# Kernel optimization log

Measured on AMD Instinct MI355X. Metric: run time of the kernel, lower is better.

## Reference

```python
import jax, jax.numpy as jnp
import numpy as np

EMBED_DIM = 1024
NUM_HEADS = 16
HEAD_DIM = EMBED_DIM // NUM_HEADS
BSZ, SEQ = 2, 2048


def setup_inputs() -> dict:
    key = jax.random.key(0)
    ks = jax.random.split(key, 7)
    s = 0.02  # keep logits in a sane range
    return {
        "hidden_states": jax.random.normal(ks[0], (BSZ, SEQ, EMBED_DIM), jnp.float32),
        "attention_mask": jnp.zeros((1, 1, SEQ, SEQ), jnp.float32),
        "q_w": jax.random.normal(ks[1], (2 * EMBED_DIM, EMBED_DIM), jnp.float32) * s,
        "q_b": jnp.zeros((2 * EMBED_DIM,), jnp.float32),
        "k_w": jax.random.normal(ks[2], (EMBED_DIM, EMBED_DIM), jnp.float32) * s,
        "k_b": jnp.zeros((EMBED_DIM,), jnp.float32),
        "v_w": jax.random.normal(ks[3], (EMBED_DIM, EMBED_DIM), jnp.float32) * s,
        "v_b": jnp.zeros((EMBED_DIM,), jnp.float32),
        "o_w": jax.random.normal(ks[4], (EMBED_DIM, EMBED_DIM), jnp.float32) * s,
        "o_b": jnp.zeros((EMBED_DIM,), jnp.float32),
    }


def reference(hidden_states, attention_mask, q_w, q_b, k_w, k_b, v_w, v_b, o_w, o_b):
    bsz, seq, _ = hidden_states.shape
    h, d = NUM_HEADS, HEAD_DIM
    inv_sqrt_d = 1.0 / np.sqrt(d).astype(np.float32)

    qg = hidden_states @ q_w.T + q_b                      # [b, s, 2*h*d]
    q, gate_logits = jnp.split(qg, [h * d], axis=-1)       # elementwise gate
    k = hidden_states @ k_w.T + k_b
    v = hidden_states @ v_w.T + v_b

    q = q.reshape(bsz, seq, h, d).transpose(0, 2, 1, 3)    # [b, h, s, d]
    k = k.reshape(bsz, seq, h, d).transpose(0, 2, 1, 3)
    v = v.reshape(bsz, seq, h, d).transpose(0, 2, 1, 3)

    scores = jnp.einsum("bhqd,bhkd->bhqk", q, k) * inv_sqrt_d
    scores = scores + attention_mask
    weights = jax.nn.softmax(scores, axis=-1)
    attn = jnp.einsum("bhqk,bhkd->bhqd", weights, v)       # [b, h, s, d]

    gate = jax.nn.sigmoid(gate_logits.reshape(bsz, seq, h, d).transpose(0, 2, 1, 3))
    attn = attn * gate

    attn = attn.transpose(0, 2, 1, 3).reshape(bsz, seq, h * d)
    return attn @ o_w.T + o_b
```

## Files before the change

kernel.cpp:

```cpp
#include <hip/hip_runtime.h>
#include <cstdint>
#include <cstddef>

#define AS1 __attribute__((address_space(1)))
#define AS3 __attribute__((address_space(3)))

typedef __bf16 bf16x8 __attribute__((ext_vector_type(8)));
typedef __bf16 bf16x4 __attribute__((ext_vector_type(4)));
typedef float  f32x4  __attribute__((ext_vector_type(4)));
typedef float  f32x16 __attribute__((ext_vector_type(16)));
typedef unsigned int u32x4 __attribute__((ext_vector_type(4)));

#define MFMA_BF16(a, b, c) __builtin_amdgcn_mfma_f32_16x16x32_bf16((a), (b), (c), 0, 0, 0)
#define MFMA32(a, b, c)    __builtin_amdgcn_mfma_f32_32x32x16_bf16((a), (b), (c), 0, 0, 0)

__device__ __forceinline__ void gload16(const __bf16* g, __bf16* l) {
  __builtin_amdgcn_global_load_lds((AS1 void*)(uintptr_t)g, (AS3 void*)l, 16, 0, 0);
}

__device__ __forceinline__ unsigned int cvtpk_bf16(float lo, float hi) {
  unsigned int r;
  asm("v_cvt_pk_bf16_f32 %0, %1, %2" : "=v"(r) : "v"(lo), "v"(hi));
  return r;
}

__device__ __forceinline__ void permswap(unsigned int& a, unsigned int& b) {
  asm volatile("v_permlane32_swap_b32 %0, %1" : "+v"(a), "+v"(b));
}

__global__ void cvt_all_kernel(
    const float* __restrict__ hs, const float* __restrict__ qw, const float* __restrict__ kw,
    const float* __restrict__ vw, const float* __restrict__ ow,
    __bf16* __restrict__ Xb, __bf16* __restrict__ qwb, __bf16* __restrict__ kwb,
    __bf16* __restrict__ vwb, __bf16* __restrict__ owb,
    const unsigned long long* __restrict__ mask, int* __restrict__ flag)
{
  const int gid = blockIdx.x * blockDim.x + threadIdx.x;
  const int stride = gridDim.x * blockDim.x;
  for (int i = gid; i < 1179648; i += stride) {
    const float* s; __bf16* d; int o;
    if (i < 524288)       { s = hs; d = Xb;  o = i; }
    else if (i < 786432)  { s = qw; d = qwb; o = i - 524288; }
    else if (i < 917504)  { s = kw; d = kwb; o = i - 786432; }
    else if (i < 1048576) { s = vw; d = vwb; o = i - 917504; }
    else                  { s = ow; d = owb; o = i - 1048576; }
    const float4* p = (const float4*)(s + (size_t)o * 8);
    float4 a = p[0], b = p[1];
    bf16x8 v;
    v[0] = (__bf16)a.x; v[1] = (__bf16)a.y; v[2] = (__bf16)a.z; v[3] = (__bf16)a.w;
    v[4] = (__bf16)b.x; v[5] = (__bf16)b.y; v[6] = (__bf16)b.z; v[7] = (__bf16)b.w;
    *(bf16x8*)(d + (size_t)o * 8) = v;
  }
  bool nz = false;
  for (int i = gid; i < 2097152; i += stride) nz |= (mask[i] != 0ull);
  if (nz) atomicOr(flag, 1);
}

__global__ __launch_bounds__(256) void proj_kernel(
    const __bf16* __restrict__ X,
    const __bf16* __restrict__ qw, const float* __restrict__ qb,
    const __bf16* __restrict__ kw, const float* __restrict__ kb,
    const __bf16* __restrict__ vw, const float* __restrict__ vb,
    __bf16* __restrict__ Qo, __bf16* __restrict__ Ko,
    __bf16* __restrict__ VTo, __bf16* __restrict__ Go)
{
  __shared__ __bf16 As[2][128][64];
  __shared__ __bf16 Bs[2][128][64];

  const int bid = blockIdx.x;
  const int r = bid >> 3;
  const int ntile = (bid & 7) * 4 + (r >> 5);
  const int mtile = r & 31;
  const int m0 = mtile * 128;
  const int n0 = ntile * 128;

  const __bf16* W; const float* bias; int nb;
  if (n0 < 2048)      { W = qw; bias = qb; nb = n0; }
  else if (n0 < 3072) { W = kw; bias = kb; nb = n0 - 2048; }
  else                { W = vw; bias = vb; nb = n0 - 3072; }

  const int tid = threadIdx.x;
  const int wv = tid >> 6, ln = tid & 63;
  const int wr = wv >> 1, wc = wv & 1;
  const int qr = ln & 15, qg = ln >> 4;
  const int lrow = ln >> 3, lcol = (ln & 7) * 8;

  f32x4 acc[4][4];
#pragma unroll
  for (int m = 0; m < 4; ++m)
#pragma unroll
    for (int n = 0; n < 4; ++n) acc[m][n] = 0.f;

  __bf16 (*Asc)[64] = As[0], (*Asn)[64] = As[1];
  __bf16 (*Bsc)[64] = Bs[0], (*Bsn)[64] = Bs[1];

#pragma unroll
  for (int i = 0; i < 4; ++i) {
    const int rb = i * 32 + wv * 8;
    gload16(X + (size_t)(m0 + rb + lrow) * 1024 + lcol, &Asc[rb][0]);
    gload16(W + (size_t)(nb + rb + lrow) * 1024 + lcol, &Bsc[rb][0]);
  }
  __syncthreads();

  for (int t = 0; t < 16; ++t) {
    if (t < 15) {
      const int k0 = (t + 1) * 64;
#pragma unroll
      for (int i = 0; i < 4; ++i) {
        const int rb = i * 32 + wv * 8;
        gload16(X + (size_t)(m0 + rb + lrow) * 1024 + k0 + lcol, &Asn[rb][0]);
        gload16(W + (size_t)(nb + rb + lrow) * 1024 + k0 + lcol, &Bsn[rb][0]);
      }
    }
#pragma unroll
    for (int kk = 0; kk < 2; ++kk) {
      bf16x8 af[4], bfv[4];
#pragma unroll
      for (int m = 0; m < 4; ++m) af[m] = *(const bf16x8*)&Asc[wr * 64 + m * 16 + qr][kk * 32 + qg * 8];
#pragma unroll
      for (int n = 0; n < 4; ++n) bfv[n] = *(const bf16x8*)&Bsc[wc * 64 + n * 16 + qr][kk * 32 + qg * 8];
#pragma unroll
      for (int m = 0; m < 4; ++m)
#pragma unroll
        for (int n = 0; n < 4; ++n) acc[m][n] = MFMA_BF16(af[m], bfv[n], acc[m][n]);
    }
    __syncthreads();
    __bf16 (*ta)[64] = Asc; Asc = Asn; Asn = ta;
    __bf16 (*tb)[64] = Bsc; Bsc = Bsn; Bsn = tb;
  }

#pragma unroll
  for (int m = 0; m < 4; ++m) {
    const int gm0 = m0 + wr * 64 + m * 16 + qg * 4;
    const int b = gm0 >> 11;
    const int s = gm0 & 2047;
#pragma unroll
    for (int n = 0; n < 4; ++n) {
      const int nl = wc * 64 + n * 16 + qr;
      const float bb = bias[nb + nl];
      if (n0 < 1024) {
        const int col = n0 + nl, hh = col >> 6, dd = col & 63;
        __bf16* dst = Qo + ((size_t)((b << 4) + hh)) * 131072 + (size_t)s * 64 + dd;
#pragma unroll
        for (int rr = 0; rr < 4; ++rr) dst[(size_t)rr * 64] = (__bf16)((acc[m][n][rr] + bb) * 0.125f);
      } else if (n0 < 2048) {
        const int j = n0 - 1024 + nl;
        __bf16* dst = Go + (size_t)gm0 * 1024 + j;
#pragma unroll
        for (int rr = 0; rr < 4; ++rr) {
          const float v = acc[m][n][rr] + bb;
          dst[(size_t)rr * 1024] = (__bf16)(1.f / (1.f + __expf(-v)));
        }
      } else if (n0 < 3072) {
        const int j = n0 - 2048 + nl, hh = j >> 6, dd = j & 63;
        __bf16* dst = Ko + ((size_t)((b << 4) + hh)) * 131072 + (size_t)s * 64 + dd;
#pragma unroll
        for (int rr = 0; rr < 4; ++rr) dst[(size_t)rr * 64] = (__bf16)(acc[m][n][rr] + bb);
      } else {
        const int j = n0 - 3072 + nl, hh = j >> 6, dd = j & 63;
        bf16x4 pv;
#pragma unroll
        for (int rr = 0; rr < 4; ++rr) pv[rr] = (__bf16)(acc[m][n][rr] + bb);
        *(bf16x4*)(VTo + ((size_t)((b << 4) + hh)) * 131072 + (size_t)dd * 2048 + s) = pv;
      }
    }
  }
}

__global__ __launch_bounds__(256, 2) void attn_kernel(
    const __bf16* __restrict__ Qb, const __bf16* __restrict__ Kb,
    const __bf16* __restrict__ VT, const __bf16* __restrict__ G,
    const float* __restrict__ mask, const int* __restrict__ flag,
    __bf16* __restrict__ attn)
{
  __shared__ __bf16 Ksh[2][32][128];
  __shared__ __bf16 Vsh[2][32][128];

  const int bid = blockIdx.x;
  const int y = bid >> 3;
  const int hl = (bid & 7) * 4 + (y >> 4);
  const int tid = threadIdx.x;
  const int w = tid >> 6;
  const int ln = tid & 63;
  const int lq = ln & 31;
  const int hi = ln >> 5;
  const int q0 = (y & 15) * 128 + w * 32;
  const int b = hl >> 4, h = hl & 15;

  const __bf16* Qh = Qb + (size_t)hl * 131072;
  const __bf16* Kh = Kb + (size_t)hl * 131072;
  const __bf16* Vh = VT + (size_t)hl * 131072;

  int kco[2], vco[2], ldst[2];
#pragma unroll
  for (int i = 0; i < 2; ++i) {
    const int prow = w * 8 + i * 4 + (ln >> 4);
    const int bphys = (ln & 15) * 16;
    const int blog = bphys ^ ((prow & 15) << 4);
    const int half = blog >> 7;
    const int col = (blog & 127) >> 1;
    kco[i] = (half * 32 + prow) * 64 + col;
    vco[i] = (half * 32 + prow) * 2048 + col;
    ldst[i] = (w * 8 + i * 4) * 256;
  }
  const int swz = (lq & 15) << 4;
  const int krow = lq * 256;

  bf16x8 qf[4];
#pragma unroll
  for (int ks = 0; ks < 4; ++ks)
    qf[ks] = *(const bf16x8*)(Qh + (size_t)(q0 + lq) * 64 + ks * 16 + hi * 8);

  f32x16 o0, o1;
#pragma unroll
  for (int i = 0; i < 16; ++i) { o0[i] = 0.f; o1[i] = 0.f; }
  float mrun = -1e30f, lrun = 0.f;

  const bool um = (*flag) != 0;

  char* Kc = (char*)&Ksh[0][0][0];  char* Kn = (char*)&Ksh[1][0][0];
  char* Vc = (char*)&Vsh[0][0][0];  char* Vn = (char*)&Vsh[1][0][0];

#pragma unroll
  for (int i = 0; i < 2; ++i) {
    gload16(Kh + kco[i], (__bf16*)(Kc + ldst[i]));
    gload16(Vh + vco[i], (__bf16*)(Vc + ldst[i]));
  }
  __syncthreads();

  for (int c = 0; c < 32; ++c) {
    const int kv0 = c * 64;
    if (c < 31) {
      const int kvn = kv0 + 64;
#pragma unroll
      for (int i = 0; i < 2; ++i) {
        gload16(Kh + kvn * 64 + kco[i], (__bf16*)(Kn + ldst[i]));
        gload16(Vh + kvn + vco[i],      (__bf16*)(Vn + ldst[i]));
      }
    }

#pragma unroll
    for (int s32 = 0; s32 < 2; ++s32) {
      bf16x8 kf[4];
#pragma unroll
      for (int ks = 0; ks < 4; ++ks)
        kf[ks] = *(const bf16x8*)(Kc + krow + ((s32 * 128 + ks * 32 + hi * 16) ^ swz));

      f32x16 s;
#pragma unroll
      for (int i = 0; i < 16; ++i) s[i] = 0.f;
#pragma unroll
      for (int ks = 0; ks < 4; ++ks) s = MFMA32(kf[ks], qf[ks], s);

      float p[16];
#pragma unroll
      for (int i = 0; i < 16; ++i) p[i] = s[i];

      if (um) {
        const size_t mrow = (size_t)(q0 + lq) * 2048 + kv0 + s32 * 32;
#pragma unroll
        for (int i = 0; i < 16; ++i)
          p[i] += mask[mrow + (i & 3) + 8 * (i >> 2) + 4 * hi];
      }

      float t = p[0];
#pragma unroll
      for (int i = 1; i < 16; ++i) t = fmaxf(t, p[i]);
      t = fmaxf(t, __shfl_xor(t, 32));
      const float mn = fmaxf(mrun, t);
      const float alpha = __expf(mrun - mn);
      mrun = mn;

      float ps = 0.f;
#pragma unroll
      for (int i = 0; i < 16; ++i) { p[i] = __expf(p[i] - mn); ps += p[i]; }
      ps += __shfl_xor(ps, 32);
      lrun = lrun * alpha + ps;

#pragma unroll
      for (int i = 0; i < 16; ++i) { o0[i] *= alpha; o1[i] *= alpha; }

      bf16x8 pa[2];
#pragma unroll
      for (int ks = 0; ks < 2; ++ks) {
        unsigned int c0 = cvtpk_bf16(p[8 * ks + 0], p[8 * ks + 1]);
        unsigned int c1 = cvtpk_bf16(p[8 * ks + 2], p[8 * ks + 3]);
        unsigned int c2 = cvtpk_bf16(p[8 * ks + 4], p[8 * ks + 5]);
        unsigned int c3 = cvtpk_bf16(p[8 * ks + 6], p[8 * ks + 7]);
        permswap(c0, c2);
        permswap(c1, c3);
        u32x4 wv; wv.x = c0; wv.y = c1; wv.z = c2; wv.w = c3;
        pa[ks] = __builtin_bit_cast(bf16x8, wv);
      }

#pragma unroll
      for (int ks = 0; ks < 2; ++ks) {
        const int kvb = s32 * 64 + ks * 32 + hi * 16;
        bf16x8 v0 = *(const bf16x8*)(Vc + krow + ((0 + kvb) ^ swz));
        bf16x8 v1 = *(const bf16x8*)(Vc + krow + ((128 + kvb) ^ swz));
        o0 = MFMA32(v0, pa[ks], o0);
        o1 = MFMA32(v1, pa[ks], o1);
      }
    }
    __syncthreads();
    char* tk = Kc; Kc = Kn; Kn = tk;
    char* tv = Vc; Vc = Vn; Vn = tv;
  }

  const float inv = 1.f / lrun;
  const size_t base = ((size_t)(b * 2048 + q0 + lq)) * 1024 + h * 64;
#pragma unroll
  for (int half = 0; half < 2; ++half) {
#pragma unroll
    for (int g = 0; g < 4; ++g) {
      const int d0 = half * 32 + g * 8 + hi * 4;
      bf16x4 g4 = *(const bf16x4*)(G + base + d0);
      bf16x4 r4;
#pragma unroll
      for (int j = 0; j < 4; ++j) {
        const float ov = half ? o1[g * 4 + j] : o0[g * 4 + j];
        r4[j] = (__bf16)(ov * inv * (float)g4[j]);
      }
      *(bf16x4*)(attn + base + d0) = r4;
    }
  }
}

__global__ __launch_bounds__(256) void oproj_kernel(
    const __bf16* __restrict__ A, const __bf16* __restrict__ ow,
    const float* __restrict__ ob, float* __restrict__ C)
{
  __shared__ __bf16 As[2][128][64];
  __shared__ __bf16 Bs[2][128][64];
  const int bid = blockIdx.x;
  const int ntile = bid & 7;
  const int mtile = bid >> 3;
  const int m0 = mtile * 128, n0 = ntile * 128;

  const int tid = threadIdx.x;
  const int wv = tid >> 6, ln = tid & 63;
  const int wr = wv >> 1, wc = wv & 1;
  const int qr = ln & 15, qg = ln >> 4;
  const int lrow = ln >> 3, lcol = (ln & 7) * 8;

  f32x4 acc[4][4];
#pragma unroll
  for (int m = 0; m < 4; ++m)
#pragma unroll
    for (int n = 0; n < 4; ++n) acc[m][n] = 0.f;

  __bf16 (*Asc)[64] = As[0], (*Asn)[64] = As[1];
  __bf16 (*Bsc)[64] = Bs[0], (*Bsn)[64] = Bs[1];

#pragma unroll
  for (int i = 0; i < 4; ++i) {
    const int rb = i * 32 + wv * 8;
    gload16(A  + (size_t)(m0 + rb + lrow) * 1024 + lcol, &Asc[rb][0]);
    gload16(ow + (size_t)(n0 + rb + lrow) * 1024 + lcol, &Bsc[rb][0]);
  }
  __syncthreads();

  for (int t = 0; t < 16; ++t) {
    if (t < 15) {
      const int k0 = (t + 1) * 64;
#pragma unroll
      for (int i = 0; i < 4; ++i) {
        const int rb = i * 32 + wv * 8;
        gload16(A  + (size_t)(m0 + rb + lrow) * 1024 + k0 + lcol, &Asn[rb][0]);
        gload16(ow + (size_t)(n0 + rb + lrow) * 1024 + k0 + lcol, &Bsn[rb][0]);
      }
    }
#pragma unroll
    for (int kk = 0; kk < 2; ++kk) {
      bf16x8 af[4], bfv[4];
#pragma unroll
      for (int m = 0; m < 4; ++m) af[m] = *(const bf16x8*)&Asc[wr * 64 + m * 16 + qr][kk * 32 + qg * 8];
#pragma unroll
      for (int n = 0; n < 4; ++n) bfv[n] = *(const bf16x8*)&Bsc[wc * 64 + n * 16 + qr][kk * 32 + qg * 8];
#pragma unroll
      for (int m = 0; m < 4; ++m)
#pragma unroll
        for (int n = 0; n < 4; ++n) acc[m][n] = MFMA_BF16(af[m], bfv[n], acc[m][n]);
    }
    __syncthreads();
    __bf16 (*ta)[64] = Asc; Asc = Asn; Asn = ta;
    __bf16 (*tb)[64] = Bsc; Bsc = Bsn; Bsn = tb;
  }

#pragma unroll
  for (int m = 0; m < 4; ++m) {
    const int gm0 = m0 + wr * 64 + m * 16 + qg * 4;
#pragma unroll
    for (int n = 0; n < 4; ++n) {
      const int gn = n0 + wc * 64 + n * 16 + qr;
      const float bb = ob[gn];
      float* dst = C + (size_t)gm0 * 1024 + gn;
#pragma unroll
      for (int rr = 0; rr < 4; ++rr) dst[(size_t)rr * 1024] = acc[m][n][rr] + bb;
    }
  }
}

extern "C" void kernel_launch(void* const* d_in, const int* in_sizes, int n_in,
                              void* d_out, int out_size, void* d_ws, size_t ws_size,
                              hipStream_t stream)
{
  const float* hs   = (const float*)d_in[0];
  const float* mask = (const float*)d_in[1];
  const float* qw   = (const float*)d_in[2];
  const float* qb   = (const float*)d_in[3];
  const float* kw   = (const float*)d_in[4];
  const float* kb   = (const float*)d_in[5];
  const float* vw   = (const float*)d_in[6];
  const float* vb   = (const float*)d_in[7];
  const float* ow   = (const float*)d_in[8];
  const float* ob   = (const float*)d_in[9];
  float* out = (float*)d_out;

  char* w = (char*)d_ws;
  int*    flag = (int*)w;
  __bf16* Xb  = (__bf16*)(w + 256);
  __bf16* qwb = Xb  + 4194304;
  __bf16* kwb = qwb + 2097152;
  __bf16* vwb = kwb + 1048576;
  __bf16* owb = vwb + 1048576;
  __bf16* Qo  = owb + 1048576;
  __bf16* Ko  = Qo  + 4194304;
  __bf16* VTo = Ko  + 4194304;
  __bf16* Go  = VTo + 4194304;
  __bf16* At  = Go  + 4194304;

  hipMemsetAsync(flag, 0, sizeof(int), stream);
  cvt_all_kernel<<<2048, 256, 0, stream>>>(hs, qw, kw, vw, ow, Xb, qwb, kwb, vwb, owb,
                                           (const unsigned long long*)mask, flag);
  proj_kernel<<<1024, 256, 0, stream>>>(Xb, qwb, qb, kwb, kb, vwb, vb, Qo, Ko, VTo, Go);
  attn_kernel<<<512, 256, 0, stream>>>(Qo, Ko, VTo, Go, mask, flag, At);
  oproj_kernel<<<256, 256, 0, stream>>>(At, owb, ob, out);
}
```

Before: 153.4 us.

## Use exp2 softmax with lazy rescaling and MFMA priority hints in attention

Folds log2(e) into the Q scaling and mask so the softmax can use the native v_exp_f32 base-2 instruction instead of __expf. Skips the running-max rescale of the output accumulators unless the max grows by more than a threshold, and defers the cross-lane row-sum reduction to the end. Adds s_setprio around MFMA sections to favor matrix issue across waves. This cuts per-tile VALU and transcendental work, at the cost of unnormalized probabilities up to 2^8 being cast to bf16, with a small precision risk.

Measured after the change: 150.0 us. -2.2%, faster.

```diff
diff --git a/kernel.cpp b/kernel.cpp
--- a/kernel.cpp
+++ b/kernel.cpp
@@ -27,6 +27,14 @@
 __device__ __forceinline__ void permswap(unsigned int& a, unsigned int& b) {
   asm volatile("v_permlane32_swap_b32 %0, %1" : "+v"(a), "+v"(b));
 }
+
+__device__ __forceinline__ float exp2_fast(float x) {
+  float r;
+  asm("v_exp_f32 %0, %1" : "=v"(r) : "v"(x));
+  return r;
+}
+
+#define LOG2E 1.4426950408889634f
 
 __global__ void cvt_all_kernel(
     const float* __restrict__ hs, const float* __restrict__ qw, const float* __restrict__ kw,
@@ -142,7 +150,7 @@
         const int col = n0 + nl, hh = col >> 6, dd = col & 63;
         __bf16* dst = Qo + ((size_t)((b << 4) + hh)) * 131072 + (size_t)s * 64 + dd;
 #pragma unroll
-        for (int rr = 0; rr < 4; ++rr) dst[(size_t)rr * 64] = (__bf16)((acc[m][n][rr] + bb) * 0.125f);
+        for (int rr = 0; rr < 4; ++rr) dst[(size_t)rr * 64] = (__bf16)((acc[m][n][rr] + bb) * (0.125f * LOG2E));
       } else if (n0 < 2048) {
         const int j = n0 - 1024 + nl;
         __bf16* dst = Go + (size_t)gm0 * 1024 + j;
@@ -249,36 +257,44 @@
       f32x16 s;
 #pragma unroll
       for (int i = 0; i < 16; ++i) s[i] = 0.f;
+      __builtin_amdgcn_s_setprio(1);
 #pragma unroll
       for (int ks = 0; ks < 4; ++ks) s = MFMA32(kf[ks], qf[ks], s);
+      __builtin_amdgcn_s_setprio(0);
 
       float p[16];
-#pragma unroll
-      for (int i = 0; i < 16; ++i) p[i] = s[i];
-
       if (um) {
         const size_t mrow = (size_t)(q0 + lq) * 2048 + kv0 + s32 * 32;
 #pragma unroll
         for (int i = 0; i < 16; ++i)
-          p[i] += mask[mrow + (i & 3) + 8 * (i >> 2) + 4 * hi];
-      }
-
-      float t = p[0];
-#pragma unroll
-      for (int i = 1; i < 16; ++i) t = fmaxf(t, p[i]);
+          p[i] = s[i] + mask[mrow + (i & 3) + 8 * (i >> 2) + 4 * hi] * LOG2E;
+      } else {
+#pragma unroll
+        for (int i = 0; i < 16; ++i) p[i] = s[i];
+      }
+
+      float t = fmaxf(fmaxf(p[0], p[1]), p[2]);
+      t = fmaxf(fmaxf(t, p[3]), p[4]);
+      t = fmaxf(fmaxf(t, p[5]), p[6]);
+      t = fmaxf(fmaxf(t, p[7]), p[8]);
+      t = fmaxf(fmaxf(t, p[9]), p[10]);
+      t = fmaxf(fmaxf(t, p[11]), p[12]);
+      t = fmaxf(fmaxf(t, p[13]), p[14]);
+      t = fmaxf(t, p[15]);
       t = fmaxf(t, __shfl_xor(t, 32));
-      const float mn = fmaxf(mrun, t);
-      const float alpha = __expf(mrun - mn);
-      mrun = mn;
+
+      if (t > mrun + 8.f) {
+        const float al = exp2_fast(mrun - t);
+        mrun = t;
+        lrun *= al;
+#pragma unroll
+        for (int i = 0; i < 16; ++i) { o0[i] *= al; o1[i] *= al; }
+      }
 
       float ps = 0.f;
 #pragma unroll
-      for (int i = 0; i < 16; ++i) { p[i] = __expf(p[i] - mn); ps += p[i]; }
-      ps += __shfl_xor(ps, 32);
-      lrun = lrun * alpha + ps;
-
-#pragma unroll
-      for (int i = 0; i < 16; ++i) { o0[i] *= alpha; o1[i] *= alpha; }
+      for (int i = 0; i < 16; ++i) { p[i] = exp2_fast(p[i] - mrun); ps += p[i]; }
+      lrun += ps;
 
       bf16x8 pa[2];
 #pragma unroll
@@ -293,6 +309,7 @@
         pa[ks] = __builtin_bit_cast(bf16x8, wv);
       }
 
+      __builtin_amdgcn_s_setprio(1);
 #pragma unroll
       for (int ks = 0; ks < 2; ++ks) {
         const int kvb = s32 * 64 + ks * 32 + hi * 16;
@@ -301,12 +318,14 @@
         o0 = MFMA32(v0, pa[ks], o0);
         o1 = MFMA32(v1, pa[ks], o1);
       }
+      __builtin_amdgcn_s_setprio(0);
     }
     __syncthreads();
     char* tk = Kc; Kc = Kn; Kn = tk;
     char* tv = Vc; Vc = Vn; Vn = tv;
   }
 
+  lrun += __shfl_xor(lrun, 32);
   const float inv = 1.f / lrun;
   const size_t base = ((size_t)(b * 2048 + q0 + lq)) * 1024 + h * 64;
 #pragma unroll
```
